# Performance work log

Hardware: AMD Instinct MI355X
Metric: run time of the kernel (lower is better)

Reference implementation:

```python
import jax, jax.numpy as jnp
import numpy as np

N_VOCAB = 50000
V_SUPPORT = 20000
D = 300
H = 512
B = 8192


def setup_inputs() -> dict:
    key = jax.random.key(0)
    ks = jax.random.split(key, 8)
    ws = jax.random.randint(ks[0], (B,), 0, N_VOCAB, dtype=jnp.int64 if jax.config.jax_enable_x64 else jnp.int32)
    cs = jax.random.randint(ks[1], (B,), 0, N_VOCAB, dtype=ws.dtype)
    vectors = jax.random.normal(ks[2], (N_VOCAB, D), dtype=jnp.float32)
    W1 = jax.random.normal(ks[3], (D, H), dtype=jnp.float32) * (1.0 / np.sqrt(D))
    b1 = jnp.zeros((H,), dtype=jnp.float32)
    W2 = jax.random.normal(ks[4], (H, V_SUPPORT), dtype=jnp.float32) * (1.0 / np.sqrt(H))
    b2 = jnp.zeros((V_SUPPORT,), dtype=jnp.float32)
    vector_to_support = jax.random.randint(ks[5], (N_VOCAB,), 0, V_SUPPORT, dtype=ws.dtype)
    return {"ws": ws, "cs": cs, "vectors": vectors, "W1": W1, "b1": b1,
            "W2": W2, "b2": b2, "vector_to_support": vector_to_support}


def reference(ws, cs, vectors, W1, b1, W2, b2, vector_to_support):
    # embedding lookup of context vectors: [B, D]
    v_c = vectors[cs]
    # FeedForward: Linear -> ReLU -> Linear, then LogSoftmax over support
    h = jax.nn.relu(v_c @ W1 + b1)            # [B, H]
    logits = h @ W2 + b2                       # [B, V]
    logp = jax.nn.log_softmax(logits, axis=-1) # [B, V]
    # map target word (vocab index) -> support index, gather per-row logprob.
    # Original does outputs.T[idx].diag() (O(B^2)); the fused equivalent is a
    # per-row gather: logp[arange(B), idx].
    w_sup = vector_to_support[ws]              # [B]
    logprobs = jnp.take_along_axis(logp, w_sup[:, None], axis=-1)[:, 0]
    return -logprobs                            # [B] NLL per example
```

## Files before the change

### kernel.cpp

```cpp
#include <hip/hip_runtime.h>
#include <hip/hip_bf16.h>
#include <hip/hip_fp8.h>
#include <math.h>


typedef __bf16 bf16x8 __attribute__((ext_vector_type(8)));
typedef float f32x4 __attribute__((ext_vector_type(4)));
typedef int i32x4 __attribute__((ext_vector_type(4)));
typedef int i32x8 __attribute__((ext_vector_type(8)));

#define B_N 8192
#define D_N 300
#define K1K 320
#define H_N 512
#define V_N 20000
#define V_PAD 20480
#define NSPLIT 16
#define SPLIT_V 1280
#define NCH 40
#define ROWS_BLK 128
#define CHUNK_BYTES 16384

#define OFF_PART (8388608u)
#define OFF_W1T  (OFF_PART + 16u*8192u*8u)
#define OFF_B2L  (OFF_W1T + 512u*320u*2u)
#define OFF_H8   (OFF_B2L + 20480u*4u)
#define OFF_W2T8 (OFF_H8 + 8192u*512u)

#define SCALE1 0x7F7F7F7F
#define LOG2E  1.4426950408889634f

__device__ inline unsigned short f2bf(float f) {
  __hip_bfloat16 h = __float2bfloat16(f);
  return *reinterpret_cast<unsigned short*>(&h);
}

__device__ inline unsigned char f2fp8(float f) {
  __hip_fp8_e4m3 q(f);
  return (unsigned char)q.__x;
}

__device__ inline float fp82f(unsigned char b) {
  __hip_fp8_e4m3 q; q.__x = b;
  return (float)q;
}

__device__ __forceinline__ void gl16(const void* g, void* l) {
  __builtin_amdgcn_global_load_lds(
      (const __attribute__((address_space(1))) void*)g,
      (__attribute__((address_space(3))) void*)l, 16, 0, 0);
}

__global__ __launch_bounds__(256) void kprep(
    const float* __restrict__ W2, unsigned long long* __restrict__ W2T8u,
    const float* __restrict__ W1, unsigned int* __restrict__ W1Tu,
    const float* __restrict__ b2, float* __restrict__ b2l)
{
  __shared__ float tile[64][65];
  const int bid = blockIdx.x;
  const int tid = threadIdx.x;

  if (bid < 2560) {
    const int n0 = (bid >> 3) * 64;
    const int k0 = (bid & 7) * 64;
    #pragma unroll
    for (int it = 0; it < 16; ++it) {
      int idx = it * 256 + tid;
      int i = idx >> 6;
      int j = idx & 63;
      float v = 0.f;
      if (n0 + j < V_N) v = W2[(size_t)(k0 + i) * V_N + n0 + j];
      tile[i][j] = v;
    }
    __syncthreads();
    #pragma unroll
    for (int it = 0; it < 2; ++it) {
      int idx = it * 256 + tid;
      int nl = idx >> 3;
      int g8 = (idx & 7) * 8;
      int n = n0 + nl;
      unsigned long long pack = 0;
      #pragma unroll
      for (int j = 0; j < 8; ++j)
        pack |= (unsigned long long)f2fp8(tile[g8 + j][nl]) << (8 * j);
      unsigned kk = (unsigned)(k0 + g8);
      unsigned off = ((unsigned)n * 512u + (kk ^ (((unsigned)n & 15u) << 4)));
      W2T8u[off >> 3] = pack;
    }
  } else if (bid < 2600) {
    const int idx0 = bid - 2560;
    const int n0 = (idx0 & 7) * 64;
    const int k0 = (idx0 >> 3) * 64;
    #pragma unroll
    for (int it = 0; it < 16; ++it) {
      int idx = it * 256 + tid;
      int i = idx >> 6;
      int j = idx & 63;
      float v = 0.f;
      if (k0 + i < D_N) v = W1[(size_t)(k0 + i) * H_N + n0 + j];
      tile[i][j] = v;
    }
    __syncthreads();
    #pragma unroll
    for (int it = 0; it < 8; ++it) {
      int idx = it * 256 + tid;
      int nl = idx >> 5;
      int k = (idx & 31) * 2;
      unsigned int lo = f2bf(tile[k][nl]);
      unsigned int hi = f2bf(tile[k + 1][nl]);
      W1Tu[((size_t)(n0 + nl) * K1K + k0 + k) >> 1] = (hi << 16) | lo;
    }
  } else {
    int i = (bid - 2600) * 256 + tid;
    if (i < V_PAD) b2l[i] = (i < V_N) ? b2[i] * LOG2E : -3.0e37f;
  }
}

__global__ __launch_bounds__(256) void k1_hidden(
    const int* __restrict__ cs, const float* __restrict__ vectors,
    const unsigned short* __restrict__ W1T,
    const float* __restrict__ b1, unsigned char* __restrict__ h8Out)
{
  __shared__ __align__(16) unsigned short vca[16][328];
  __shared__ int rowIdx[16];
  const int tid = threadIdx.x;
  const int lane = tid & 63;
  const int w = tid >> 6;
  const int l15 = lane & 15;
  const int l4 = lane >> 4;
  const int r0 = blockIdx.x * 16;
  if (tid < 16) rowIdx[tid] = cs[r0 + tid];
  __syncthreads();
  for (int idx = tid; idx < 16 * 328; idx += 256) {
    int r = idx / 328;
    int k = idx - r * 328;
    float v = (k < D_N) ? vectors[(size_t)rowIdx[r] * D_N + k] : 0.f;
    vca[r][k] = f2bf(v);
  }
  __syncthreads();

  bf16x8 afr[10];
  #pragma unroll
  for (int t = 0; t < 10; ++t)
    afr[t] = *(const bf16x8*)&vca[l15][t * 32 + l4 * 8];

  f32x4 acc[8];
  #pragma unroll
  for (int ct = 0; ct < 8; ++ct) acc[ct] = (f32x4){0.f, 0.f, 0.f, 0.f};

  #pragma unroll
  for (int t = 0; t < 10; ++t) {
    #pragma unroll
    for (int ct = 0; ct < 8; ++ct) {
      const int n = w * 128 + ct * 16 + l15;
      bf16x8 bfr = *(const bf16x8*)(W1T + (size_t)n * K1K + t * 32 + l4 * 8);
      acc[ct] = __builtin_amdgcn_mfma_f32_16x16x32_bf16(afr[t], bfr, acc[ct], 0, 0, 0);
    }
  }

  #pragma unroll
  for (int ct = 0; ct < 8; ++ct) {
    const int n = w * 128 + ct * 16 + l15;
    const float bb = b1[n];
    #pragma unroll
    for (int r = 0; r < 4; ++r) {
      const int row = r0 + l4 * 4 + r;
      h8Out[(size_t)row * H_N + n] = f2fp8(fmaxf(acc[ct][r] + bb, 0.f));
    }
  }
}

__device__ __forceinline__ void stage_chunk(const char* g, char* l, int tid) {
  #pragma unroll
  for (int it = 0; it < 4; ++it) {
    const unsigned o = (unsigned)tid * 16 + it * 4096;
    gl16(g + o, l + o);
  }
}

__global__ __launch_bounds__(256, 4) void k3_fused(
    const unsigned char* __restrict__ h8,
    const char* __restrict__ W2T8,
    const float* __restrict__ b2l,
    float2* __restrict__ partOut)
{
  __shared__ __align__(16) char smB[2 * CHUNK_BYTES];
  __shared__ float b2s[SPLIT_V];
  const int tid = threadIdx.x;
  const int lane = tid & 63;
  const int w = tid >> 6;
  const int l15 = lane & 15;
  const int l4 = lane >> 4;
  const int s = blockIdx.x & 15;
  const int rb = blockIdx.x >> 4;
  const int r0 = rb * ROWS_BLK + w * 32;
  const char* gsplit = W2T8 + (size_t)s * SPLIT_V * 512;
  const int sCol = s * SPLIT_V;

  i32x8 afr[2][4];
  #pragma unroll
  for (int m = 0; m < 2; ++m) {
    const unsigned char* ap = h8 + (size_t)(r0 + m * 16 + l15) * H_N + l4 * 32;
    #pragma unroll
    for (int t = 0; t < 4; ++t) {
      i32x4 lo = *(const i32x4*)(ap + t * 128);
      i32x4 hi = *(const i32x4*)(ap + t * 128 + 16);
      afr[m][t] = __builtin_shufflevector(lo, hi, 0, 1, 2, 3, 4, 5, 6, 7);
    }
  }

  float s_run[8];
  #pragma unroll
  for (int ri = 0; ri < 8; ++ri) s_run[ri] = 0.f;

  for (int i = tid; i < SPLIT_V; i += 256) b2s[i] = b2l[sCol + i];

  stage_chunk(gsplit, smB, tid);

  const unsigned swz = (unsigned)l15 << 4;

  #pragma unroll 1
  for (int c = 0; c < NCH; ++c) {
    asm volatile("s_waitcnt vmcnt(0) lgkmcnt(0)" ::: "memory");
    __builtin_amdgcn_s_barrier();

    char* cur = smB + (c & 1) * CHUNK_BYTES;
    if (c + 1 < NCH)
      stage_chunk(gsplit + (size_t)(c + 1) * CHUNK_BYTES,
                  smB + ((c & 1) ^ 1) * CHUNK_BYTES, tid);

    f32x4 acc[2][2];
    #pragma unroll
    for (int m = 0; m < 2; ++m)
      #pragma unroll
      for (int ct = 0; ct < 2; ++ct) acc[m][ct] = (f32x4){0.f, 0.f, 0.f, 0.f};

    #pragma unroll
    for (int t = 0; t < 4; ++t) {
      #pragma unroll
      for (int ct = 0; ct < 2; ++ct) {
        const char* bp = cur + (ct * 16 + l15) * 512;
        i32x4 lo = *(const i32x4*)(bp + (((unsigned)(t * 128 + l4 * 32)) ^ swz));
        i32x4 hi = *(const i32x4*)(bp + (((unsigned)(t * 128 + l4 * 32 + 16)) ^ swz));
        i32x8 bfr = __builtin_shufflevector(lo, hi, 0, 1, 2, 3, 4, 5, 6, 7);
        __builtin_amdgcn_s_setprio(1);
        acc[0][ct] = __builtin_amdgcn_mfma_scale_f32_16x16x128_f8f6f4(
            afr[0][t], bfr, acc[0][ct], 0, 0, 0, SCALE1, 0, SCALE1);
        acc[1][ct] = __builtin_amdgcn_mfma_scale_f32_16x16x128_f8f6f4(
            afr[1][t], bfr, acc[1][ct], 0, 0, 0, SCALE1, 0, SCALE1);
        __builtin_amdgcn_s_setprio(0);
      }
    }

    const float b2c0 = b2s[c * 32 + l15];
    const float b2c1 = b2s[c * 32 + 16 + l15];
    #pragma unroll
    for (int m = 0; m < 2; ++m)
      #pragma unroll
      for (int r = 0; r < 4; ++r) {
        const int ri = m * 4 + r;
        float f0 = fmaf(acc[m][0][r], LOG2E, b2c0);
        float f1 = fmaf(acc[m][1][r], LOG2E, b2c1);
        s_run[ri] += __builtin_amdgcn_exp2f(f0) + __builtin_amdgcn_exp2f(f1);
      }
  }

  #pragma unroll
  for (int m = 0; m < 2; ++m)
    #pragma unroll
    for (int r = 0; r < 4; ++r) {
      int ri = m * 4 + r;
      float sc = s_run[ri];
      #pragma unroll
      for (int k = 1; k < 16; k <<= 1) sc += __shfl_xor(sc, k);
      if (l15 == 0) {
        int grow = r0 + m * 16 + l4 * 4 + r;
        partOut[(size_t)s * B_N + grow] = make_float2(0.f, sc);
      }
    }
}

__global__ __launch_bounds__(256) void k45_final(
    const unsigned char* __restrict__ h8, const char* __restrict__ W2T8,
    const float* __restrict__ b2, const int* __restrict__ wsIdx,
    const int* __restrict__ v2s, const float2* __restrict__ part,
    float* __restrict__ out)
{
  const int row = blockIdx.x * 4 + (threadIdx.x >> 6);
  const int lane = threadIdx.x & 63;
  const int tc = v2s[wsIdx[row]];
  unsigned long long hv = *(const unsigned long long*)(h8 + (size_t)row * H_N + lane * 8);
  const unsigned off = ((unsigned)(lane * 8)) ^ (((unsigned)tc & 15u) << 4);
  unsigned long long wv = *(const unsigned long long*)(W2T8 + (size_t)tc * 512 + off);
  float sdot = 0.f;
  #pragma unroll
  for (int j = 0; j < 8; ++j)
    sdot += fp82f((unsigned char)(hv >> (8 * j))) * fp82f((unsigned char)(wv >> (8 * j)));
  #pragma unroll
  for (int k = 32; k >= 1; k >>= 1) sdot += __shfl_xor(sdot, k);
  if (lane == 0) {
    const float tgt = sdot + b2[tc];
    float S = 0.f;
    #pragma unroll
    for (int s = 0; s < NSPLIT; ++s) S += part[(size_t)s * B_N + row].y;
    out[row] = logf(S) - tgt;
  }
}

extern "C" void kernel_launch(void* const* d_in, const int* in_sizes, int n_in,
                              void* d_out, int out_size, void* d_ws, size_t ws_size,
                              hipStream_t stream) {
  const int*   wsIdx   = (const int*)d_in[0];
  const int*   cs      = (const int*)d_in[1];
  const float* vectors = (const float*)d_in[2];
  const float* W1      = (const float*)d_in[3];
  const float* b1      = (const float*)d_in[4];
  const float* W2      = (const float*)d_in[5];
  const float* b2      = (const float*)d_in[6];
  const int*   v2s     = (const int*)d_in[7];

  char* wsb = (char*)d_ws;
  float2* part = (float2*)(wsb + OFF_PART);
  unsigned short* W1T = (unsigned short*)(wsb + OFF_W1T);
  float*  b2l  = (float*)(wsb + OFF_B2L);
  unsigned char* h8   = (unsigned char*)(wsb + OFF_H8);
  char*   W2T8 = wsb + OFF_W2T8;
  float*  out  = (float*)d_out;

  hipLaunchKernelGGL(kprep, dim3(2680), dim3(256), 0, stream,
                     W2, (unsigned long long*)W2T8, W1, (unsigned int*)W1T, b2, b2l);
  hipLaunchKernelGGL(k1_hidden, dim3(B_N / 16), dim3(256), 0, stream, cs, vectors, W1T, b1, h8);
  hipLaunchKernelGGL(k3_fused, dim3((B_N / ROWS_BLK) * NSPLIT), dim3(256), 0, stream,
                     h8, W2T8, b2l, part);
  hipLaunchKernelGGL(k45_final, dim3(B_N / 4), dim3(256), 0, stream,
                     h8, W2T8, b2, wsIdx, v2s, part, out);
}
```

Measured before the change: 125.2 us.

## Software-pipeline exp epilogue of previous chunk with current chunk MFMAs

Double-buffers the MFMA accumulators so the exp2/sum epilogue for chunk c-1 is interleaved with the MFMA work for chunk c, letting the transcendental VALU work overlap the matrix pipe. The first phase consumes a dummy accumulator with a very negative bias so its contribution is zero. Launch bounds occupancy is lowered from 4 to 3 waves to leave room for the extra accumulator registers, which trades occupancy for instruction-level overlap.

Result: slower. 165.8 us (+32.5%).

```diff
diff --git a/kernel.cpp b/kernel.cpp
--- a/kernel.cpp
+++ b/kernel.cpp
@@ -178,7 +178,50 @@
   }
 }
 
-__global__ __launch_bounds__(256, 4) void k3_fused(
+
+#define CHUNK_PHASE(c, accC, b2c0v, b2c1v, accP, b2p0v, b2p1v)                 \
+  {                                                                            \
+    asm volatile("s_waitcnt vmcnt(0) lgkmcnt(0)" ::: "memory");                \
+    __builtin_amdgcn_s_barrier();                                              \
+    char* cur = smB + ((c) & 1) * CHUNK_BYTES;                                 \
+    if ((c) + 1 < NCH)                                                         \
+      stage_chunk(gsplit + (size_t)((c) + 1) * CHUNK_BYTES,                    \
+                  smB + (((c) & 1) ^ 1) * CHUNK_BYTES, tid);                   \
+    b2c0v = b2s[(c) * 32 + l15];                                               \
+    b2c1v = b2s[(c) * 32 + 16 + l15];                                          \
+    _Pragma("unroll")                                                          \
+    for (int m_ = 0; m_ < 2; ++m_)                                             \
+      _Pragma("unroll")                                                        \
+      for (int ct_ = 0; ct_ < 2; ++ct_)                                        \
+        accC[m_][ct_] = (f32x4){0.f, 0.f, 0.f, 0.f};                           \
+    _Pragma("unroll")                                                          \
+    for (int t_ = 0; t_ < 4; ++t_) {                                           \
+      _Pragma("unroll")                                                        \
+      for (int ct_ = 0; ct_ < 2; ++ct_) {                                      \
+        const char* bp = cur + (ct_ * 16 + l15) * 512;                         \
+        i32x4 lo = *(const i32x4*)(bp + (((unsigned)(t_*128 + l4*32)) ^ swz)); \
+        i32x4 hi = *(const i32x4*)(bp + (((unsigned)(t_*128 + l4*32 + 16)) ^ swz)); \
+        i32x8 bfr = __builtin_shufflevector(lo, hi, 0, 1, 2, 3, 4, 5, 6, 7);   \
+        __builtin_amdgcn_s_setprio(1);                                         \
+        accC[0][ct_] = __builtin_amdgcn_mfma_scale_f32_16x16x128_f8f6f4(       \
+            afr[0][t_], bfr, accC[0][ct_], 0, 0, 0, SCALE1, 0, SCALE1);        \
+        accC[1][ct_] = __builtin_amdgcn_mfma_scale_f32_16x16x128_f8f6f4(       \
+            afr[1][t_], bfr, accC[1][ct_], 0, 0, 0, SCALE1, 0, SCALE1);        \
+        __builtin_amdgcn_s_setprio(0);                                         \
+      }                                                                        \
+        \
+      _Pragma("unroll")                                                        \
+      for (int r2_ = 0; r2_ < 2; ++r2_) {                                      \
+        const int ri_ = t_ * 2 + r2_;                                \
+        const int m_ = ri_ >> 2, r_ = ri_ & 3;                                 \
+        float f0_ = fmaf(accP[m_][0][r_], LOG2E, b2p0v);                       \
+        float f1_ = fmaf(accP[m_][1][r_], LOG2E, b2p1v);                       \
+        s_run[ri_] += __builtin_amdgcn_exp2f(f0_) + __builtin_amdgcn_exp2f(f1_);\
+      }                                                                        \
+    }                                                                          \
+  }
+
+__global__ __launch_bounds__(256, 3) void k3_fused(
     const unsigned char* __restrict__ h8,
     const char* __restrict__ W2T8,
     const float* __restrict__ b2l,
@@ -219,51 +262,29 @@
 
   const unsigned swz = (unsigned)l15 << 4;
 
+  f32x4 accA[2][2], accB[2][2];
+  #pragma unroll
+  for (int m = 0; m < 2; ++m)
+    #pragma unroll
+    for (int ct = 0; ct < 2; ++ct) accB[m][ct] = (f32x4){0.f, 0.f, 0.f, 0.f};
+  float b2A0, b2A1;
+  float b2B0 = -3.0e37f, b2B1 = -3.0e37f;
+
   #pragma unroll 1
-  for (int c = 0; c < NCH; ++c) {
-    asm volatile("s_waitcnt vmcnt(0) lgkmcnt(0)" ::: "memory");
-    __builtin_amdgcn_s_barrier();
-
-    char* cur = smB + (c & 1) * CHUNK_BYTES;
-    if (c + 1 < NCH)
-      stage_chunk(gsplit + (size_t)(c + 1) * CHUNK_BYTES,
-                  smB + ((c & 1) ^ 1) * CHUNK_BYTES, tid);
-
-    f32x4 acc[2][2];
-    #pragma unroll
-    for (int m = 0; m < 2; ++m)
-      #pragma unroll
-      for (int ct = 0; ct < 2; ++ct) acc[m][ct] = (f32x4){0.f, 0.f, 0.f, 0.f};
-
-    #pragma unroll
-    for (int t = 0; t < 4; ++t) {
-      #pragma unroll
-      for (int ct = 0; ct < 2; ++ct) {
-        const char* bp = cur + (ct * 16 + l15) * 512;
-        i32x4 lo = *(const i32x4*)(bp + (((unsigned)(t * 128 + l4 * 32)) ^ swz));
-        i32x4 hi = *(const i32x4*)(bp + (((unsigned)(t * 128 + l4 * 32 + 16)) ^ swz));
-        i32x8 bfr = __builtin_shufflevector(lo, hi, 0, 1, 2, 3, 4, 5, 6, 7);
-        __builtin_amdgcn_s_setprio(1);
-        acc[0][ct] = __builtin_amdgcn_mfma_scale_f32_16x16x128_f8f6f4(
-            afr[0][t], bfr, acc[0][ct], 0, 0, 0, SCALE1, 0, SCALE1);
-        acc[1][ct] = __builtin_amdgcn_mfma_scale_f32_16x16x128_f8f6f4(
-            afr[1][t], bfr, acc[1][ct], 0, 0, 0, SCALE1, 0, SCALE1);
-        __builtin_amdgcn_s_setprio(0);
-      }
-    }
-
-    const float b2c0 = b2s[c * 32 + l15];
-    const float b2c1 = b2s[c * 32 + 16 + l15];
-    #pragma unroll
-    for (int m = 0; m < 2; ++m)
-      #pragma unroll
-      for (int r = 0; r < 4; ++r) {
-        const int ri = m * 4 + r;
-        float f0 = fmaf(acc[m][0][r], LOG2E, b2c0);
-        float f1 = fmaf(acc[m][1][r], LOG2E, b2c1);
-        s_run[ri] += __builtin_amdgcn_exp2f(f0) + __builtin_amdgcn_exp2f(f1);
-      }
-  }
+  for (int i = 0; i < NCH / 2; ++i) {
+    CHUNK_PHASE(2 * i,     accA, b2A0, b2A1, accB, b2B0, b2B1);
+    CHUNK_PHASE(2 * i + 1, accB, b2B0, b2B1, accA, b2A0, b2A1);
+  }
+
+  #pragma unroll
+  for (int m = 0; m < 2; ++m)
+    #pragma unroll
+    for (int r = 0; r < 4; ++r) {
+      const int ri = m * 4 + r;
+      float f0 = fmaf(accB[m][0][r], LOG2E, b2B0);
+      float f1 = fmaf(accB[m][1][r], LOG2E, b2B1);
+      s_run[ri] += __builtin_amdgcn_exp2f(f0) + __builtin_amdgcn_exp2f(f1);
+    }
 
   #pragma unroll
   for (int m = 0; m < 2; ++m)
```
